# Kernel optimization log

Hardware: AMD Instinct MI355X
Metric: run time of the kernel (lower is better)

The kernel has to match this reference:

```python
import jax, jax.numpy as jnp
import numpy as np

N_NODES = 50000
N_EDGES = 800000
D_IN = 256
D_HID = 256
D_OUT = 256


def sage_conv(x, src, dst, W_l, b_l, W_r, num_nodes):
    """PyG SAGEConv with mean aggregation: lin_l(mean_{j in N(i)} x_j) + lin_r(x_i)."""
    msg = x[src]  # [E, C] gather of source-node features
    agg = jax.ops.segment_sum(msg, dst, num_segments=num_nodes)  # [N, C]
    cnt = jax.ops.segment_sum(jnp.ones((src.shape[0],), x.dtype), dst,
                              num_segments=num_nodes)
    mean = agg / jnp.maximum(cnt, 1.0)[:, None]  # isolated nodes -> 0
    return mean @ W_l.T + b_l + x @ W_r.T


def setup_inputs() -> dict:
    key = jax.random.key(0)
    ks = jax.random.split(key, 10)
    s = 1.0 / np.sqrt(D_IN)
    x = jax.random.normal(ks[0], (N_NODES, D_IN), dtype=jnp.float32)
    edge_index = jax.random.randint(ks[1], (2, N_EDGES), 0, N_NODES, dtype=jnp.int64)
    mention_index = jax.random.randint(ks[2], (1,), 0, N_NODES, dtype=jnp.int64)
    return {
        "x": x,
        "edge_index": edge_index,
        "mention_index": mention_index,
        "W1_l": jax.random.uniform(ks[3], (D_HID, D_IN), jnp.float32, -s, s),
        "b1_l": jnp.zeros((D_HID,), jnp.float32),
        "W1_r": jax.random.uniform(ks[4], (D_HID, D_IN), jnp.float32, -s, s),
        "W2_l": jax.random.uniform(ks[5], (D_OUT, D_HID), jnp.float32, -s, s),
        "b2_l": jnp.zeros((D_OUT,), jnp.float32),
        "W2_r": jax.random.uniform(ks[6], (D_OUT, D_HID), jnp.float32, -s, s),
    }


def reference(x, edge_index, mention_index, W1_l, b1_l, W1_r, W2_l, b2_l, W2_r):
    src, dst = edge_index[0], edge_index[1]
    h = jax.nn.relu(sage_conv(x, src, dst, W1_l, b1_l, W1_r, N_NODES))
    h = sage_conv(h, src, dst, W2_l, b2_l, W2_r, N_NODES)
    # dropout in the original is a no-op (result discarded)
    logits = (h[mention_index] * h).sum(axis=1)  # [N]
    z = jax.nn.softmax(logits, axis=0)
    return z
```

## Files before the change

kernel.cpp:

```cpp
#include <hip/hip_runtime.h>
#include <math.h>

#define N_NODES 50000
#define N_EDGES 800000
#define D 256
#define K2 512
#define M_PAD 50048
#define BM 128
#define BN 256
#define BK 32
#define SCAN_B 196

typedef __attribute__((ext_vector_type(8))) short short8;
typedef __attribute__((ext_vector_type(8))) unsigned short ushort8;
typedef __attribute__((ext_vector_type(4))) float floatx4;

__device__ __forceinline__ unsigned short bf16_rn(float f) {
    union { float f; unsigned u; } a; a.f = f;
    unsigned r = a.u + 0x7FFF + ((a.u >> 16) & 1);
    return (unsigned short)(r >> 16);
}
__device__ __forceinline__ float bf16_to_f(unsigned short h) {
    union { unsigned u; float f; } a; a.u = ((unsigned)h) << 16;
    return a.f;
}
__device__ __forceinline__ void load_lds16(const void* g, void* lds) {
    __builtin_amdgcn_global_load_lds((const __attribute__((address_space(1))) void*)g,
                                     (__attribute__((address_space(3))) void*)lds, 16, 0, 0);
}

__global__ void k_count(const int* __restrict__ dst, int* __restrict__ deg) {
    int e = blockIdx.x * blockDim.x + threadIdx.x;
    if (e < N_EDGES) atomicAdd(&deg[dst[e]], 1);
}

__global__ void k_scan1(const int* __restrict__ deg, int* __restrict__ bsum) {
    __shared__ int red[256];
    int b = blockIdx.x, t = threadIdx.x;
    int i = b * 256 + t;
    red[t] = (i < N_NODES) ? deg[i] : 0;
    __syncthreads();
    for (int o = 128; o; o >>= 1) {
        if (t < o) red[t] += red[t + o];
        __syncthreads();
    }
    if (t == 0) bsum[b] = red[0];
}

__global__ void k_scan2(const int* __restrict__ bsum, int* __restrict__ boff) {
    __shared__ int sh[256];
    int t = threadIdx.x;
    sh[t] = (t < SCAN_B) ? bsum[t] : 0;
    __syncthreads();
    for (int o = 1; o < 256; o <<= 1) {
        int v = (t >= o) ? sh[t - o] : 0;
        __syncthreads();
        sh[t] += v;
        __syncthreads();
    }
    boff[t] = (t == 0) ? 0 : sh[t - 1];
}

__global__ void k_scan3(const int* __restrict__ deg, const int* __restrict__ boff,
                        int* __restrict__ cursor) {
    __shared__ int sh[256];
    int b = blockIdx.x, t = threadIdx.x;
    int i = b * 256 + t;
    int v = (i < N_NODES) ? deg[i] : 0;
    sh[t] = v;
    __syncthreads();
    for (int o = 1; o < 256; o <<= 1) {
        int val = (t >= o) ? sh[t - o] : 0;
        __syncthreads();
        sh[t] += val;
        __syncthreads();
    }
    if (i < N_NODES) cursor[i] = boff[b] + sh[t] - v;
}

__global__ void k_bucket(const int* __restrict__ src, const int* __restrict__ dst,
                         int* __restrict__ cursor, int* __restrict__ csr_src) {
    int e = blockIdx.x * blockDim.x + threadIdx.x;
    if (e >= N_EDGES) return;
    int pos = atomicAdd(&cursor[dst[e]], 1);
    csr_src[pos] = src[e];
}

__global__ void k_splitX(const float* __restrict__ x, unsigned short* __restrict__ Ahi,
                         unsigned short* __restrict__ Alo) {
    int t = blockIdx.x * blockDim.x + threadIdx.x;
    if (t >= N_NODES * 64) return;
    int m = t >> 6, j = (t & 63) * 4;
    float4 v = *(const float4*)&x[(size_t)m * D + j];
    ushort4 hi, lo;
    hi.x = bf16_rn(v.x); lo.x = bf16_rn(v.x - bf16_to_f(hi.x));
    hi.y = bf16_rn(v.y); lo.y = bf16_rn(v.y - bf16_to_f(hi.y));
    hi.z = bf16_rn(v.z); lo.z = bf16_rn(v.z - bf16_to_f(hi.z));
    hi.w = bf16_rn(v.w); lo.w = bf16_rn(v.w - bf16_to_f(hi.w));
    *(ushort4*)&Ahi[(size_t)m * K2 + 256 + j] = hi;
    *(ushort4*)&Alo[(size_t)m * K2 + 256 + j] = lo;
}

__global__ void k_splitB(const float* __restrict__ Wl, const float* __restrict__ Wr,
                         unsigned short* __restrict__ Bhi, unsigned short* __restrict__ Blo) {
    int t = blockIdx.x * blockDim.x + threadIdx.x;
    if (t >= 256 * 128) return;
    int n = t >> 7, k = (t & 127) * 4;
    const float* srcp = (k < 256) ? &Wl[(size_t)n * 256 + k] : &Wr[(size_t)n * 256 + k - 256];
    float4 v = *(const float4*)srcp;
    ushort4 hi, lo;
    hi.x = bf16_rn(v.x); lo.x = bf16_rn(v.x - bf16_to_f(hi.x));
    hi.y = bf16_rn(v.y); lo.y = bf16_rn(v.y - bf16_to_f(hi.y));
    hi.z = bf16_rn(v.z); lo.z = bf16_rn(v.z - bf16_to_f(hi.z));
    hi.w = bf16_rn(v.w); lo.w = bf16_rn(v.w - bf16_to_f(hi.w));
    *(ushort4*)&Bhi[(size_t)n * K2 + k] = hi;
    *(ushort4*)&Blo[(size_t)n * K2 + k] = lo;
}

__global__ __launch_bounds__(256) void k_agg(const int* __restrict__ cursor,
                                             const int* __restrict__ deg,
                                             const int* __restrict__ csr,
                                             unsigned short* __restrict__ Ahi,
                                             unsigned short* __restrict__ Alo) {
    int node = blockIdx.x * 4 + (threadIdx.x >> 6);
    int lane = threadIdx.x & 63;
    if (node >= N_NODES) return;
    int d = deg[node], end = cursor[node], start = end - d;
    int h = lane >> 5;
    int col = (lane & 31) * 8;
    float acc0[8] = {}, acc1[8] = {};
    int j = start;
    for (; j + 4 <= end; j += 4) {
        int i0 = csr[j + h];
        int i1 = csr[j + 2 + h];
        ushort8 v0 = *(const ushort8*)&Ahi[(size_t)i0 * K2 + 256 + col];
        ushort8 v1 = *(const ushort8*)&Ahi[(size_t)i1 * K2 + 256 + col];
        #pragma unroll
        for (int k = 0; k < 8; k++) {
            acc0[k] += bf16_to_f(v0[k]);
            acc1[k] += bf16_to_f(v1[k]);
        }
    }
    if (j + 2 <= end) {
        int i0 = csr[j + h];
        ushort8 v0 = *(const ushort8*)&Ahi[(size_t)i0 * K2 + 256 + col];
        #pragma unroll
        for (int k = 0; k < 8; k++) acc0[k] += bf16_to_f(v0[k]);
        j += 2;
    }
    if (j < end && h == 0) {
        int i0 = csr[j];
        ushort8 v0 = *(const ushort8*)&Ahi[(size_t)i0 * K2 + 256 + col];
        #pragma unroll
        for (int k = 0; k < 8; k++) acc0[k] += bf16_to_f(v0[k]);
    }
    float inv = 1.0f / fmaxf((float)d, 1.0f);
    ushort8 hi, lo;
    #pragma unroll
    for (int k = 0; k < 8; k++) {
        float a = acc0[k] + acc1[k];
        a += __shfl_xor(a, 32);
        float m = a * inv;
        hi[k] = bf16_rn(m);
        lo[k] = bf16_rn(m - bf16_to_f(hi[k]));
    }
    if (h == 0) {
        *(ushort8*)&Ahi[(size_t)node * K2 + col] = hi;
        *(ushort8*)&Alo[(size_t)node * K2 + col] = lo;
    }
}

__global__ __launch_bounds__(256) void k_small(const int* __restrict__ mention,
                                               const int* __restrict__ deg,
                                               const int* __restrict__ cursor,
                                               const int* __restrict__ csr,
                                               const float* __restrict__ x,
                                               const float* __restrict__ W1l,
                                               const float* __restrict__ W1r,
                                               const float* __restrict__ b1,
                                               float* __restrict__ h1m) {
    int m = mention[0];
    int dm = min(deg[m], 255);
    int slot = blockIdx.x;
    if (slot > dm) return;
    int startm = cursor[m] - deg[m];
    int node = (slot == 0) ? m : csr[startm + slot - 1];
    __shared__ float smean[D], sx[D];
    int t = threadIdx.x;
    int d = deg[node], end = cursor[node], start = end - d;
    float a = 0.f;
    for (int j = start; j < end; j++) a += x[(size_t)csr[j] * D + t];
    smean[t] = a / fmaxf((float)d, 1.0f);
    sx[t] = x[(size_t)node * D + t];
    __syncthreads();
    float z = b1[t];
    for (int k = 0; k < D; k++)
        z += smean[k] * W1l[(size_t)t * D + k] + sx[k] * W1r[(size_t)t * D + k];
    h1m[(size_t)slot * D + t] = fmaxf(z, 0.f);
}

__global__ __launch_bounds__(256) void k_vu(const int* __restrict__ mention,
                                            const int* __restrict__ deg,
                                            const float* __restrict__ h1m,
                                            const float* __restrict__ W2l,
                                            const float* __restrict__ W2r,
                                            const float* __restrict__ b2,
                                            float* __restrict__ u,
                                            float* __restrict__ cout) {
    __shared__ float sm[D], sh[D], sv[D], red[256];
    int m = mention[0];
    int dm = min(deg[m], 255);
    int t = threadIdx.x;
    float a = 0.f;
    for (int j = 1; j <= dm; j++) a += h1m[(size_t)j * D + t];
    sm[t] = a / fmaxf((float)deg[m], 1.0f);
    sh[t] = h1m[t];
    __syncthreads();
    float acc = b2[t];
    for (int k = 0; k < D; k++)
        acc += sm[k] * W2l[(size_t)t * D + k] + sh[k] * W2r[(size_t)t * D + k];
    sv[t] = acc;
    red[t] = b2[t] * acc;
    __syncthreads();
    for (int o = 128; o; o >>= 1) {
        if (t < o) red[t] += red[t + o];
        __syncthreads();
    }
    if (t == 0) cout[0] = red[0];
    float a1 = 0.f, a2 = 0.f;
    for (int n = 0; n < D; n++) {
        a1 += W2l[(size_t)n * D + t] * sv[n];
        a2 += W2r[(size_t)n * D + t] * sv[n];
    }
    u[t] = a1;
    u[D + t] = a2;
}

__global__ __launch_bounds__(512, 4)
void k_gemm_fused(const unsigned short* __restrict__ Ahi,
                  const unsigned short* __restrict__ Alo,
                  const unsigned short* __restrict__ Bhi,
                  const unsigned short* __restrict__ Blo,
                  const float* __restrict__ bias,
                  const float* __restrict__ u,
                  float* __restrict__ s,
                  float* __restrict__ t_) {
    __shared__ unsigned short sA[2][BM * BK];
    __shared__ unsigned short sB[2][BN * BK];
    __shared__ float sred[BM], tred[BM];
    int tid = threadIdx.x;
    int br = blockIdx.x;
    int lane = tid & 63, wv = tid >> 6;
    int wm = (wv >> 2) * 64, wn = (wv & 3) * 64;
    int q = lane >> 4, r = lane & 15;

    float biasv[4], u1v[4], u2v[4];
    #pragma unroll
    for (int nt = 0; nt < 4; nt++) {
        int gc = wn + nt * 16 + r;
        biasv[nt] = bias[gc];
        u1v[nt] = u[gc];
        u2v[nt] = u[256 + gc];
    }
    if (tid < BM) { sred[tid] = 0.f; tred[tid] = 0.f; }

    floatx4 acc[4][4] = {};

    const size_t arow0 = (size_t)br * BM;
    int seg = lane & 3;
    int rl16 = lane >> 2;

    for (int kt = 0; kt < K2 / BK; kt++) {
        {
            int rloc = wv * 16 + rl16;
            size_t gA = (arow0 + rloc) * (size_t)K2 + kt * BK + seg * 8;
            int ldsoff = (wv * 16) * BK;
            load_lds16(Ahi + gA, &sA[0][ldsoff]);
            load_lds16(Alo + gA, &sA[1][ldsoff]);
        }
        #pragma unroll
        for (int t = 0; t < 2; t++) {
            int rloc = wv * 32 + t * 16 + rl16;
            size_t gB = (size_t)rloc * K2 + kt * BK + seg * 8;
            int ldsoff = (wv * 32 + t * 16) * BK;
            load_lds16(Bhi + gB, &sB[0][ldsoff]);
            load_lds16(Blo + gB, &sB[1][ldsoff]);
        }
        __syncthreads();
        short8 ah[4], al[4], bh[4], bl[4];
        #pragma unroll
        for (int i = 0; i < 4; i++) {
            ah[i] = *(const short8*)&sA[0][(wm + i * 16 + r) * BK + q * 8];
            al[i] = *(const short8*)&sA[1][(wm + i * 16 + r) * BK + q * 8];
            bh[i] = *(const short8*)&sB[0][(wn + i * 16 + r) * BK + q * 8];
            bl[i] = *(const short8*)&sB[1][(wn + i * 16 + r) * BK + q * 8];
        }
        #pragma unroll
        for (int mt = 0; mt < 4; mt++)
            #pragma unroll
            for (int nt = 0; nt < 4; nt++) {
                acc[mt][nt] = __builtin_amdgcn_mfma_f32_16x16x32_bf16(ah[mt], bh[nt], acc[mt][nt], 0, 0, 0);
                acc[mt][nt] = __builtin_amdgcn_mfma_f32_16x16x32_bf16(ah[mt], bl[nt], acc[mt][nt], 0, 0, 0);
                acc[mt][nt] = __builtin_amdgcn_mfma_f32_16x16x32_bf16(al[mt], bh[nt], acc[mt][nt], 0, 0, 0);
            }
        __syncthreads();
    }

    #pragma unroll
    for (int mt = 0; mt < 4; mt++) {
        #pragma unroll
        for (int reg = 0; reg < 4; reg++) {
            float sacc = 0.f, tacc = 0.f;
            #pragma unroll
            for (int nt = 0; nt < 4; nt++) {
                float h = fmaxf(acc[mt][nt][reg] + biasv[nt], 0.f);
                sacc += h * u1v[nt];
                tacc += h * u2v[nt];
            }
            #pragma unroll
            for (int off = 1; off < 16; off <<= 1) {
                sacc += __shfl_xor(sacc, off);
                tacc += __shfl_xor(tacc, off);
            }
            if (r == 0) {
                int row = wm + mt * 16 + q * 4 + reg;
                atomicAdd(&sred[row], sacc);
                atomicAdd(&tred[row], tacc);
            }
        }
    }
    __syncthreads();
    if (tid < BM) {
        size_t grow = arow0 + tid;
        if (grow < N_NODES) {
            s[grow] = sred[tid];
            t_[grow] = tred[tid];
        }
    }
}

__global__ __launch_bounds__(256) void k_logits_sm1(const int* __restrict__ deg,
                                                    const int* __restrict__ cursor,
                                                    const int* __restrict__ csr,
                                                    const float* __restrict__ s,
                                                    const float* __restrict__ t_,
                                                    const float* __restrict__ cptr,
                                                    float* __restrict__ logits,
                                                    float* __restrict__ pmax,
                                                    float* __restrict__ psum) {
    __shared__ float red[256];
    int b = blockIdx.x, t = threadIdx.x;
    int i = b * 256 + t;
    float lg = -INFINITY;
    if (i < N_NODES) {
        int d = deg[i];
        int end = cursor[i];
        int start = end - d;
        float sum = 0.f;
        for (int j = start; j < end; j++) sum += s[csr[j]];
        lg = sum / fmaxf((float)d, 1.0f) + t_[i] + cptr[0];
        logits[i] = lg;
    }
    red[t] = lg;
    __syncthreads();
    for (int o = 128; o; o >>= 1) {
        if (t < o) red[t] = fmaxf(red[t], red[t + o]);
        __syncthreads();
    }
    float mb = red[0];
    __syncthreads();
    red[t] = (i < N_NODES) ? __expf(lg - mb) : 0.f;
    __syncthreads();
    for (int o = 128; o; o >>= 1) {
        if (t < o) red[t] += red[t + o];
        __syncthreads();
    }
    if (t == 0) { pmax[b] = mb; psum[b] = red[0]; }
}

__global__ void k_sm2(const float* __restrict__ pmax, const float* __restrict__ psum,
                      float* __restrict__ gS) {
    __shared__ float rm[256], rs[256];
    int t = threadIdx.x;
    float m = (t < SCAN_B) ? pmax[t] : -INFINITY;
    rm[t] = m;
    __syncthreads();
    for (int o = 128; o; o >>= 1) {
        if (t < o) rm[t] = fmaxf(rm[t], rm[t + o]);
        __syncthreads();
    }
    float g = rm[0];
    __syncthreads();
    rs[t] = (t < SCAN_B) ? psum[t] * __expf(m - g) : 0.f;
    __syncthreads();
    for (int o = 128; o; o >>= 1) {
        if (t < o) rs[t] += rs[t + o];
        __syncthreads();
    }
    if (t == 0) { gS[0] = g; gS[1] = 1.0f / rs[0]; }
}

__global__ void k_sm3(const float* __restrict__ logits, const float* __restrict__ gS,
                      float* __restrict__ out) {
    int i = blockIdx.x * blockDim.x + threadIdx.x;
    if (i < N_NODES) out[i] = __expf(logits[i] - gS[0]) * gS[1];
}

extern "C" void kernel_launch(void* const* d_in, const int* in_sizes, int n_in,
                              void* d_out, int out_size, void* d_ws, size_t ws_size,
                              hipStream_t stream) {
    const float* x   = (const float*)d_in[0];
    const int*   ei  = (const int*)d_in[1];
    const int*   src = ei;
    const int*   dst = ei + N_EDGES;
    const int*   mention = (const int*)d_in[2];
    const float* W1l = (const float*)d_in[3];
    const float* b1  = (const float*)d_in[4];
    const float* W1r = (const float*)d_in[5];
    const float* W2l = (const float*)d_in[6];
    const float* b2  = (const float*)d_in[7];
    const float* W2r = (const float*)d_in[8];

    char* w = (char*)d_ws;
    unsigned short* Ahi = (unsigned short*)w;  w += (size_t)M_PAD * K2 * 2;
    unsigned short* Alo = (unsigned short*)w;  w += (size_t)M_PAD * K2 * 2;
    unsigned short* Bhi = (unsigned short*)w;  w += (size_t)256 * K2 * 2;
    unsigned short* Blo = (unsigned short*)w;  w += (size_t)256 * K2 * 2;
    float* s     = (float*)w;  w += (size_t)N_NODES * 4;
    float* t_    = (float*)w;  w += (size_t)N_NODES * 4;
    int* deg     = (int*)w;    w += (size_t)N_NODES * 4;
    float* logit = (float*)w;  w += (size_t)N_NODES * 4;
    float* h1m   = (float*)w;  w += (size_t)256 * D * 4;
    float* u     = (float*)w;  w += 2 * D * 4;
    float* c     = (float*)w;  w += 16;
    float* pmax  = (float*)w;  w += 256 * 4;
    float* psum  = (float*)w;  w += 256 * 4;
    float* gS    = (float*)w;  w += 16;
    int* cursor  = (int*)w;    w += (size_t)N_NODES * 4;
    int* bsum    = (int*)w;    w += 256 * 4;
    int* boff    = (int*)w;    w += 256 * 4;
    int* csr     = (int*)w;    w += (size_t)N_EDGES * 4;

    hipMemsetAsync(deg, 0, (size_t)N_NODES * sizeof(int), stream);

    k_count <<<(N_EDGES + 255) / 256, 256, 0, stream>>>(dst, deg);
    k_scan1 <<<SCAN_B, 256, 0, stream>>>(deg, bsum);
    k_scan2 <<<1, 256, 0, stream>>>(bsum, boff);
    k_scan3 <<<SCAN_B, 256, 0, stream>>>(deg, boff, cursor);
    k_bucket<<<(N_EDGES + 255) / 256, 256, 0, stream>>>(src, dst, cursor, csr);

    k_splitX<<<(N_NODES * 64 + 255) / 256, 256, 0, stream>>>(x, Ahi, Alo);
    k_splitB<<<(256 * 128 + 255) / 256, 256, 0, stream>>>(W1l, W1r, Bhi, Blo);
    k_agg   <<<(N_NODES + 3) / 4, 256, 0, stream>>>(cursor, deg, csr, Ahi, Alo);

    k_small <<<256, 256, 0, stream>>>(mention, deg, cursor, csr, x, W1l, W1r, b1, h1m);
    k_vu    <<<1, 256, 0, stream>>>(mention, deg, h1m, W2l, W2r, b2, u, c);

    k_gemm_fused<<<M_PAD / BM, 512, 0, stream>>>(Ahi, Alo, Bhi, Blo, b1, u, s, t_);

    k_logits_sm1<<<SCAN_B, 256, 0, stream>>>(deg, cursor, csr, s, t_, c, logit, pmax, psum);
    k_sm2   <<<1, 256, 0, stream>>>(pmax, psum, gS);
    k_sm3   <<<(N_NODES + 255) / 256, 256, 0, stream>>>(logit, gS, (float*)d_out);
}
```

Measured before the change: 381.8 us.

## Fuse CSR build, mention MLP and softmax into cooperative grid-synced kernels

Replaces the count/scan/bucket chain, the k_small/k_vu pair and the three softmax kernels with three cooperative launches that use grid-wide syncs between phases. This cuts kernel launch count and the intermediate logits and offset buffers. Separately, the neighbor-aggregation loop is unrolled to four independent gathers per iteration to keep more loads in flight. The trade-offs are grid-sync costs, fewer blocks in the CSR kernel, and a lower cap on how many mention-node neighbors are handled explicitly (95 instead of 255).

```diff
diff --git a/kernel.cpp b/kernel.cpp
--- a/kernel.cpp
+++ b/kernel.cpp
@@ -1,5 +1,8 @@
 #include <hip/hip_runtime.h>
+#include <hip/hip_cooperative_groups.h>
 #include <math.h>
+
+namespace cg = cooperative_groups;
 
 #define N_NODES 50000
 #define N_EDGES 800000
@@ -10,6 +13,8 @@
 #define BN 256
 #define BK 32
 #define SCAN_B 196
+#define CSR_G 512
+#define CSR_CH 98
 
 typedef __attribute__((ext_vector_type(8))) short short8;
 typedef __attribute__((ext_vector_type(8))) unsigned short ushort8;
@@ -29,61 +34,58 @@
                                      (__attribute__((address_space(3))) void*)lds, 16, 0, 0);
 }
 
-__global__ void k_count(const int* __restrict__ dst, int* __restrict__ deg) {
-    int e = blockIdx.x * blockDim.x + threadIdx.x;
-    if (e < N_EDGES) atomicAdd(&deg[dst[e]], 1);
-}
-
-__global__ void k_scan1(const int* __restrict__ deg, int* __restrict__ bsum) {
+__global__ __launch_bounds__(256) void k_csr(const int* __restrict__ src,
+                                             const int* __restrict__ dst,
+                                             int* __restrict__ deg,
+                                             int* __restrict__ cursor,
+                                             int* __restrict__ bsum,
+                                             int* __restrict__ csr_src) {
+    cg::grid_group g = cg::this_grid();
     __shared__ int red[256];
     int b = blockIdx.x, t = threadIdx.x;
-    int i = b * 256 + t;
-    red[t] = (i < N_NODES) ? deg[i] : 0;
+    int tid = b * 256 + t;
+    const int NT = CSR_G * 256;
+    for (int e = tid; e < N_EDGES; e += NT) atomicAdd(&deg[dst[e]], 1);
+    g.sync();
+    int base = b * CSR_CH;
+    int lim = min(base + CSR_CH, N_NODES);
+    int ssum = 0;
+    for (int i = base + t; i < lim; i += 256) ssum += deg[i];
+    red[t] = ssum;
     __syncthreads();
     for (int o = 128; o; o >>= 1) {
         if (t < o) red[t] += red[t + o];
         __syncthreads();
     }
     if (t == 0) bsum[b] = red[0];
-}
-
-__global__ void k_scan2(const int* __restrict__ bsum, int* __restrict__ boff) {
-    __shared__ int sh[256];
-    int t = threadIdx.x;
-    sh[t] = (t < SCAN_B) ? bsum[t] : 0;
+    g.sync();
+    int partial = 0;
+    for (int i = t; i < b; i += 256) partial += bsum[i];
+    __syncthreads();
+    red[t] = partial;
+    __syncthreads();
+    for (int o = 128; o; o >>= 1) {
+        if (t < o) red[t] += red[t + o];
+        __syncthreads();
+    }
+    int boff = red[0];
+    __syncthreads();
+    int i = base + t;
+    int v = (t < CSR_CH && i < N_NODES) ? deg[i] : 0;
+    red[t] = v;
     __syncthreads();
     for (int o = 1; o < 256; o <<= 1) {
-        int v = (t >= o) ? sh[t - o] : 0;
-        __syncthreads();
-        sh[t] += v;
-        __syncthreads();
-    }
-    boff[t] = (t == 0) ? 0 : sh[t - 1];
-}
-
-__global__ void k_scan3(const int* __restrict__ deg, const int* __restrict__ boff,
-                        int* __restrict__ cursor) {
-    __shared__ int sh[256];
-    int b = blockIdx.x, t = threadIdx.x;
-    int i = b * 256 + t;
-    int v = (i < N_NODES) ? deg[i] : 0;
-    sh[t] = v;
-    __syncthreads();
-    for (int o = 1; o < 256; o <<= 1) {
-        int val = (t >= o) ? sh[t - o] : 0;
-        __syncthreads();
-        sh[t] += val;
-        __syncthreads();
-    }
-    if (i < N_NODES) cursor[i] = boff[b] + sh[t] - v;
-}
-
-__global__ void k_bucket(const int* __restrict__ src, const int* __restrict__ dst,
-                         int* __restrict__ cursor, int* __restrict__ csr_src) {
-    int e = blockIdx.x * blockDim.x + threadIdx.x;
-    if (e >= N_EDGES) return;
-    int pos = atomicAdd(&cursor[dst[e]], 1);
-    csr_src[pos] = src[e];
+        int val = (t >= o) ? red[t - o] : 0;
+        __syncthreads();
+        red[t] += val;
+        __syncthreads();
+    }
+    if (t < CSR_CH && i < N_NODES) cursor[i] = boff + red[t] - v;
+    g.sync();
+    for (int e = tid; e < N_EDGES; e += NT) {
+        int pos = atomicAdd(&cursor[dst[e]], 1);
+        csr_src[pos] = src[e];
+    }
 }
 
 __global__ void k_splitX(const float* __restrict__ x, unsigned short* __restrict__ Ahi,
@@ -128,29 +130,44 @@
     int d = deg[node], end = cursor[node], start = end - d;
     int h = lane >> 5;
     int col = (lane & 31) * 8;
-    float acc0[8] = {}, acc1[8] = {};
+    const unsigned short* Xb = Ahi + 256 + col;
+    float acc0[8] = {}, acc1[8] = {}, acc2[8] = {}, acc3[8] = {};
     int j = start;
-    for (; j + 4 <= end; j += 4) {
-        int i0 = csr[j + h];
-        int i1 = csr[j + 2 + h];
-        ushort8 v0 = *(const ushort8*)&Ahi[(size_t)i0 * K2 + 256 + col];
-        ushort8 v1 = *(const ushort8*)&Ahi[(size_t)i1 * K2 + 256 + col];
+    for (; j + 8 <= end; j += 8) {
+        int i0 = csr[j + h], i1 = csr[j + 2 + h], i2 = csr[j + 4 + h], i3 = csr[j + 6 + h];
+        ushort8 v0 = *(const ushort8*)&Xb[(size_t)i0 * K2];
+        ushort8 v1 = *(const ushort8*)&Xb[(size_t)i1 * K2];
+        ushort8 v2 = *(const ushort8*)&Xb[(size_t)i2 * K2];
+        ushort8 v3 = *(const ushort8*)&Xb[(size_t)i3 * K2];
         #pragma unroll
         for (int k = 0; k < 8; k++) {
             acc0[k] += bf16_to_f(v0[k]);
             acc1[k] += bf16_to_f(v1[k]);
-        }
+            acc2[k] += bf16_to_f(v2[k]);
+            acc3[k] += bf16_to_f(v3[k]);
+        }
+    }
+    if (j + 4 <= end) {
+        int i0 = csr[j + h], i1 = csr[j + 2 + h];
+        ushort8 v0 = *(const ushort8*)&Xb[(size_t)i0 * K2];
+        ushort8 v1 = *(const ushort8*)&Xb[(size_t)i1 * K2];
+        #pragma unroll
+        for (int k = 0; k < 8; k++) {
+            acc0[k] += bf16_to_f(v0[k]);
+            acc1[k] += bf16_to_f(v1[k]);
+        }
+        j += 4;
     }
     if (j + 2 <= end) {
         int i0 = csr[j + h];
-        ushort8 v0 = *(const ushort8*)&Ahi[(size_t)i0 * K2 + 256 + col];
+        ushort8 v0 = *(const ushort8*)&Xb[(size_t)i0 * K2];
         #pragma unroll
         for (int k = 0; k < 8; k++) acc0[k] += bf16_to_f(v0[k]);
         j += 2;
     }
     if (j < end && h == 0) {
         int i0 = csr[j];
-        ushort8 v0 = *(const ushort8*)&Ahi[(size_t)i0 * K2 + 256 + col];
+        ushort8 v0 = *(const ushort8*)&Xb[(size_t)i0 * K2];
         #pragma unroll
         for (int k = 0; k < 8; k++) acc0[k] += bf16_to_f(v0[k]);
     }
@@ -158,7 +175,7 @@
     ushort8 hi, lo;
     #pragma unroll
     for (int k = 0; k < 8; k++) {
-        float a = acc0[k] + acc1[k];
+        float a = (acc0[k] + acc1[k]) + (acc2[k] + acc3[k]);
         a += __shfl_xor(a, 32);
         float m = a * inv;
         hi[k] = bf16_rn(m);
@@ -170,70 +187,66 @@
     }
 }
 
-__global__ __launch_bounds__(256) void k_small(const int* __restrict__ mention,
-                                               const int* __restrict__ deg,
-                                               const int* __restrict__ cursor,
-                                               const int* __restrict__ csr,
-                                               const float* __restrict__ x,
-                                               const float* __restrict__ W1l,
-                                               const float* __restrict__ W1r,
-                                               const float* __restrict__ b1,
-                                               float* __restrict__ h1m) {
+__global__ __launch_bounds__(256) void k_small_vu(const int* __restrict__ mention,
+                                                  const int* __restrict__ deg,
+                                                  const int* __restrict__ cursor,
+                                                  const int* __restrict__ csr,
+                                                  const float* __restrict__ x,
+                                                  const float* __restrict__ W1l,
+                                                  const float* __restrict__ W1r,
+                                                  const float* __restrict__ b1,
+                                                  const float* __restrict__ W2l,
+                                                  const float* __restrict__ W2r,
+                                                  const float* __restrict__ b2,
+                                                  float* __restrict__ h1m,
+                                                  float* __restrict__ u,
+                                                  float* __restrict__ cout) {
+    cg::grid_group g = cg::this_grid();
+    __shared__ float s0[D], s1[D], s2[D], red[256];
     int m = mention[0];
-    int dm = min(deg[m], 255);
+    int dm = min(deg[m], (int)gridDim.x - 1);
     int slot = blockIdx.x;
-    if (slot > dm) return;
-    int startm = cursor[m] - deg[m];
-    int node = (slot == 0) ? m : csr[startm + slot - 1];
-    __shared__ float smean[D], sx[D];
     int t = threadIdx.x;
-    int d = deg[node], end = cursor[node], start = end - d;
-    float a = 0.f;
-    for (int j = start; j < end; j++) a += x[(size_t)csr[j] * D + t];
-    smean[t] = a / fmaxf((float)d, 1.0f);
-    sx[t] = x[(size_t)node * D + t];
-    __syncthreads();
-    float z = b1[t];
-    for (int k = 0; k < D; k++)
-        z += smean[k] * W1l[(size_t)t * D + k] + sx[k] * W1r[(size_t)t * D + k];
-    h1m[(size_t)slot * D + t] = fmaxf(z, 0.f);
-}
-
-__global__ __launch_bounds__(256) void k_vu(const int* __restrict__ mention,
-                                            const int* __restrict__ deg,
-                                            const float* __restrict__ h1m,
-                                            const float* __restrict__ W2l,
-                                            const float* __restrict__ W2r,
-                                            const float* __restrict__ b2,
-                                            float* __restrict__ u,
-                                            float* __restrict__ cout) {
-    __shared__ float sm[D], sh[D], sv[D], red[256];
-    int m = mention[0];
-    int dm = min(deg[m], 255);
-    int t = threadIdx.x;
-    float a = 0.f;
-    for (int j = 1; j <= dm; j++) a += h1m[(size_t)j * D + t];
-    sm[t] = a / fmaxf((float)deg[m], 1.0f);
-    sh[t] = h1m[t];
-    __syncthreads();
-    float acc = b2[t];
-    for (int k = 0; k < D; k++)
-        acc += sm[k] * W2l[(size_t)t * D + k] + sh[k] * W2r[(size_t)t * D + k];
-    sv[t] = acc;
-    red[t] = b2[t] * acc;
-    __syncthreads();
-    for (int o = 128; o; o >>= 1) {
-        if (t < o) red[t] += red[t + o];
-        __syncthreads();
-    }
-    if (t == 0) cout[0] = red[0];
-    float a1 = 0.f, a2 = 0.f;
-    for (int n = 0; n < D; n++) {
-        a1 += W2l[(size_t)n * D + t] * sv[n];
-        a2 += W2r[(size_t)n * D + t] * sv[n];
-    }
-    u[t] = a1;
-    u[D + t] = a2;
+    if (slot <= dm) {
+        int startm = cursor[m] - deg[m];
+        int node = (slot == 0) ? m : csr[startm + slot - 1];
+        int d = deg[node], end = cursor[node], start = end - d;
+        float a = 0.f;
+        for (int j = start; j < end; j++) a += x[(size_t)csr[j] * D + t];
+        s0[t] = a / fmaxf((float)d, 1.0f);
+        s1[t] = x[(size_t)node * D + t];
+        __syncthreads();
+        float z = b1[t];
+        for (int k = 0; k < D; k++)
+            z += s0[k] * W1l[(size_t)t * D + k] + s1[k] * W1r[(size_t)t * D + k];
+        h1m[(size_t)slot * D + t] = fmaxf(z, 0.f);
+    }
+    g.sync();
+    if (blockIdx.x == 0) {
+        float a = 0.f;
+        for (int j = 1; j <= dm; j++) a += h1m[(size_t)j * D + t];
+        s0[t] = a / fmaxf((float)deg[m], 1.0f);
+        s1[t] = h1m[t];
+        __syncthreads();
+        float acc = b2[t];
+        for (int k = 0; k < D; k++)
+            acc += s0[k] * W2l[(size_t)t * D + k] + s1[k] * W2r[(size_t)t * D + k];
+        s2[t] = acc;
+        red[t] = b2[t] * acc;
+        __syncthreads();
+        for (int o = 128; o; o >>= 1) {
+            if (t < o) red[t] += red[t + o];
+            __syncthreads();
+        }
+        if (t == 0) cout[0] = red[0];
+        float a1 = 0.f, a2 = 0.f;
+        for (int n = 0; n < D; n++) {
+            a1 += W2l[(size_t)n * D + t] * s2[n];
+            a2 += W2r[(size_t)n * D + t] * s2[n];
+        }
+        u[t] = a1;
+        u[D + t] = a2;
+    }
 }
 
 __global__ __launch_bounds__(512, 4)
@@ -339,15 +352,16 @@
     }
 }
 
-__global__ __launch_bounds__(256) void k_logits_sm1(const int* __restrict__ deg,
-                                                    const int* __restrict__ cursor,
-                                                    const int* __restrict__ csr,
-                                                    const float* __restrict__ s,
-                                                    const float* __restrict__ t_,
-                                                    const float* __restrict__ cptr,
-                                                    float* __restrict__ logits,
-                                                    float* __restrict__ pmax,
-                                                    float* __restrict__ psum) {
+__global__ __launch_bounds__(256) void k_logsm(const int* __restrict__ deg,
+                                               const int* __restrict__ cursor,
+                                               const int* __restrict__ csr,
+                                               const float* __restrict__ s,
+                                               const float* __restrict__ t_,
+                                               const float* __restrict__ cptr,
+                                               float* __restrict__ pmax,
+                                               float* __restrict__ psum,
+                                               float* __restrict__ out) {
+    cg::grid_group g = cg::this_grid();
     __shared__ float red[256];
     int b = blockIdx.x, t = threadIdx.x;
     int i = b * 256 + t;
@@ -359,7 +373,6 @@
         float sum = 0.f;
         for (int j = start; j < end; j++) sum += s[csr[j]];
         lg = sum / fmaxf((float)d, 1.0f) + t_[i] + cptr[0];
-        logits[i] = lg;
     }
     red[t] = lg;
     __syncthreads();
@@ -376,34 +389,25 @@
         __syncthreads();
     }
     if (t == 0) { pmax[b] = mb; psum[b] = red[0]; }
-}
-
-__global__ void k_sm2(const float* __restrict__ pmax, const float* __restrict__ psum,
-                      float* __restrict__ gS) {
-    __shared__ float rm[256], rs[256];
-    int t = threadIdx.x;
+    g.sync();
     float m = (t < SCAN_B) ? pmax[t] : -INFINITY;
-    rm[t] = m;
-    __syncthreads();
-    for (int o = 128; o; o >>= 1) {
-        if (t < o) rm[t] = fmaxf(rm[t], rm[t + o]);
-        __syncthreads();
-    }
-    float g = rm[0];
-    __syncthreads();
-    rs[t] = (t < SCAN_B) ? psum[t] * __expf(m - g) : 0.f;
-    __syncthreads();
-    for (int o = 128; o; o >>= 1) {
-        if (t < o) rs[t] += rs[t + o];
-        __syncthreads();
-    }
-    if (t == 0) { gS[0] = g; gS[1] = 1.0f / rs[0]; }
-}
-
-__global__ void k_sm3(const float* __restrict__ logits, const float* __restrict__ gS,
-                      float* __restrict__ out) {
-    int i = blockIdx.x * blockDim.x + threadIdx.x;
-    if (i < N_NODES) out[i] = __expf(logits[i] - gS[0]) * gS[1];
+    __syncthreads();
+    red[t] = m;
+    __syncthreads();
+    for (int o = 128; o; o >>= 1) {
+        if (t < o) red[t] = fmaxf(red[t], red[t + o]);
+        __syncthreads();
+    }
+    float gmax = red[0];
+    __syncthreads();
+    red[t] = (t < SCAN_B) ? psum[t] * __expf(m - gmax) : 0.f;
+    __syncthreads();
+    for (int o = 128; o; o >>= 1) {
+        if (t < o) red[t] += red[t + o];
+        __syncthreads();
+    }
+    float inv = 1.0f / red[0];
+    if (i < N_NODES) out[i] = __expf(lg - gmax) * inv;
 }
 
 extern "C" void kernel_launch(void* const* d_in, const int* in_sizes, int n_in,
@@ -429,36 +433,41 @@
     float* s     = (float*)w;  w += (size_t)N_NODES * 4;
     float* t_    = (float*)w;  w += (size_t)N_NODES * 4;
     int* deg     = (int*)w;    w += (size_t)N_NODES * 4;
-    float* logit = (float*)w;  w += (size_t)N_NODES * 4;
-    float* h1m   = (float*)w;  w += (size_t)256 * D * 4;
+    float* h1m   = (float*)w;  w += (size_t)96 * D * 4;
     float* u     = (float*)w;  w += 2 * D * 4;
     float* c     = (float*)w;  w += 16;
     float* pmax  = (float*)w;  w += 256 * 4;
     float* psum  = (float*)w;  w += 256 * 4;
-    float* gS    = (float*)w;  w += 16;
     int* cursor  = (int*)w;    w += (size_t)N_NODES * 4;
-    int* bsum    = (int*)w;    w += 256 * 4;
-    int* boff    = (int*)w;    w += 256 * 4;
+    int* bsum    = (int*)w;    w += CSR_G * 4;
     int* csr     = (int*)w;    w += (size_t)N_EDGES * 4;
 
     hipMemsetAsync(deg, 0, (size_t)N_NODES * sizeof(int), stream);
 
-    k_count <<<(N_EDGES + 255) / 256, 256, 0, stream>>>(dst, deg);
-    k_scan1 <<<SCAN_B, 256, 0, stream>>>(deg, bsum);
-    k_scan2 <<<1, 256, 0, stream>>>(bsum, boff);
-    k_scan3 <<<SCAN_B, 256, 0, stream>>>(deg, boff, cursor);
-    k_bucket<<<(N_EDGES + 255) / 256, 256, 0, stream>>>(src, dst, cursor, csr);
+    {
+        void* args[] = {(void*)&src, (void*)&dst, (void*)&deg, (void*)&cursor,
+                        (void*)&bsum, (void*)&csr};
+        hipLaunchCooperativeKernel((void*)k_csr, dim3(CSR_G), dim3(256), args, 0, stream);
+    }
 
     k_splitX<<<(N_NODES * 64 + 255) / 256, 256, 0, stream>>>(x, Ahi, Alo);
     k_splitB<<<(256 * 128 + 255) / 256, 256, 0, stream>>>(W1l, W1r, Bhi, Blo);
     k_agg   <<<(N_NODES + 3) / 4, 256, 0, stream>>>(cursor, deg, csr, Ahi, Alo);
 
-    k_small <<<256, 256, 0, stream>>>(mention, deg, cursor, csr, x, W1l, W1r, b1, h1m);
-    k_vu    <<<1, 256, 0, stream>>>(mention, deg, h1m, W2l, W2r, b2, u, c);
+    {
+        void* args[] = {(void*)&mention, (void*)&deg, (void*)&cursor, (void*)&csr,
+                        (void*)&x, (void*)&W1l, (void*)&W1r, (void*)&b1,
+                        (void*)&W2l, (void*)&W2r, (void*)&b2,
+                        (void*)&h1m, (void*)&u, (void*)&c};
+        hipLaunchCooperativeKernel((void*)k_small_vu, dim3(96), dim3(256), args, 0, stream);
+    }
 
     k_gemm_fused<<<M_PAD / BM, 512, 0, stream>>>(Ahi, Alo, Bhi, Blo, b1, u, s, t_);
 
-    k_logits_sm1<<<SCAN_B, 256, 0, stream>>>(deg, cursor, csr, s, t_, c, logit, pmax, psum);
-    k_sm2   <<<1, 256, 0, stream>>>(pmax, psum, gS);
-    k_sm3   <<<(N_NODES + 255) / 256, 256, 0, stream>>>(logit, gS, (float*)d_out);
-}
+    {
+        float* out = (float*)d_out;
+        void* args[] = {(void*)&deg, (void*)&cursor, (void*)&csr, (void*)&s, (void*)&t_,
+                        (void*)&c, (void*)&pmax, (void*)&psum, (void*)&out};
+        hipLaunchCooperativeKernel((void*)k_logsm, dim3(SCAN_B), dim3(256), args, 0, stream);
+    }
+}
```

Result: slower. 622.2 us (+63.0%).
